# Performance work log

Measured on AMD Instinct MI355X. Metric: run time of the kernel, lower is better.

Reference implementation:

```python
import jax, jax.numpy as jnp
import numpy as np


def _qkernel(r, i, j, k):
    # Build the real-valued block kernel of a quaternion dense layer.
    # r,i,j,k: [in/4, out/4] -> kernel [in, out] implementing the Hamilton product.
    col_r = jnp.concatenate([r, -i, -j, -k], axis=0)
    col_i = jnp.concatenate([i, r, -k, j], axis=0)
    col_j = jnp.concatenate([j, k, r, -i], axis=0)
    col_k = jnp.concatenate([k, -j, i, r], axis=0)
    return jnp.concatenate([col_r, col_i, col_j, col_k], axis=1)


def setup_inputs() -> dict:
    key = jax.random.key(0)
    ks = jax.random.split(key, 12)
    B, F, H = 32768, 1024, 256
    F4, H4 = F // 4, H // 4
    s_in = 1.0 / np.sqrt(F)
    s_h = 1.0 / np.sqrt(H)
    inp = {
        "x": jax.random.normal(ks[0], (B, F), dtype=jnp.float32),
        "wx_r": jax.random.normal(ks[1], (4, F4, H4), dtype=jnp.float32) * s_in,
        "wx_i": jax.random.normal(ks[2], (4, F4, H4), dtype=jnp.float32) * s_in,
        "wx_j": jax.random.normal(ks[3], (4, F4, H4), dtype=jnp.float32) * s_in,
        "wx_k": jax.random.normal(ks[4], (4, F4, H4), dtype=jnp.float32) * s_in,
        "bx": jnp.zeros((4, H), dtype=jnp.float32),
        "uh_r": jax.random.normal(ks[5], (4, H4, H4), dtype=jnp.float32) * s_h,
        "uh_i": jax.random.normal(ks[6], (4, H4, H4), dtype=jnp.float32) * s_h,
        "uh_j": jax.random.normal(ks[7], (4, H4, H4), dtype=jnp.float32) * s_h,
        "uh_k": jax.random.normal(ks[8], (4, H4, H4), dtype=jnp.float32) * s_h,
        "fco_w": jax.random.normal(ks[9], (H, H), dtype=jnp.float32) * s_h,
        "fco_b": jnp.zeros((H,), dtype=jnp.float32),
    }
    return inp


def reference(x, wx_r, wx_i, wx_j, wx_k, bx, uh_r, uh_i, uh_j, uh_k, fco_w, fco_b):
    # Single-step quaternion LSTM cell with zero initial hidden/cell state.
    # Gate order along leading axis: [forget, input, output, cell].
    Kx = jax.vmap(_qkernel)(wx_r, wx_i, wx_j, wx_k)   # [4, F, H]
    Ku = jax.vmap(_qkernel)(uh_r, uh_i, uh_j, uh_k)   # [4, H, H]
    H = bx.shape[1]
    h0 = jnp.zeros((x.shape[0], H), dtype=x.dtype)
    c0 = h0
    gx = jnp.einsum('bf,gfh->gbh', x, Kx) + bx[:, None, :]   # [4, B, H]
    gu = jnp.einsum('bh,ghk->gbk', h0, Ku)                    # [4, B, H]
    z = gx + gu
    ft = jax.nn.sigmoid(z[0])
    it = jax.nn.sigmoid(z[1])
    ot = jax.nn.sigmoid(z[2])
    at = z[3]
    c = it * jnp.tanh(at) + ft * c0
    h = ot * jnp.tanh(c)
    return h @ fco_w + fco_b
```

## Files before the change

### kernel.cpp

```cpp
#include <hip/hip_runtime.h>
#include <cstdint>
#include <cstddef>

#define WS_WP   0
#define WS_FCO  1572864
#define WS_BP   1703936
#define WS_HVP  1707008

typedef __attribute__((ext_vector_type(8))) __bf16 bf16x8;
typedef __attribute__((ext_vector_type(4))) __bf16 bf16x4;
typedef __attribute__((ext_vector_type(4))) float floatx4;

__device__ __forceinline__ unsigned short f2bf(float f) {
  unsigned int u = __builtin_bit_cast(unsigned int, f);
  u += 0x7fffu + ((u >> 16) & 1u);
  return (unsigned short)(u >> 16);
}

__device__ __forceinline__ float sigmf(float z) {
  return __builtin_amdgcn_rcpf(1.f + __expf(-z));
}
__device__ __forceinline__ float tanh_(float z) {
  return 1.f - 2.f * __builtin_amdgcn_rcpf(1.f + __expf(2.f * z));
}

__device__ __forceinline__ void gld16(const void* g, void* l) {
  __builtin_amdgcn_global_load_lds(
      (const __attribute__((address_space(1))) unsigned int*)g,
      (__attribute__((address_space(3))) unsigned int*)l, 16, 0, 0);
}

__global__ __launch_bounds__(256) void pack_k(
    const float* __restrict__ wr, const float* __restrict__ wi,
    const float* __restrict__ wj, const float* __restrict__ wk,
    const float* __restrict__ bx, const float* __restrict__ fw,
    unsigned short* __restrict__ Wp, unsigned short* __restrict__ Fp,
    float* __restrict__ bp) {
  int t = threadIdx.x;
  if (blockIdx.x < 384) {
    int gpp = blockIdx.x >> 7;
    int oct = blockIdx.x & 127;
    int gp = gpp + 1;
    int h = t;
    int hb = h >> 6, hr = h & 63;
    int f0 = oct << 3;
    int fb = f0 >> 8, fr0 = f0 & 255;
    const int   comp_t[4][4] = {{0,1,2,3},{1,0,3,2},{2,3,0,1},{3,2,1,0}};
    const float sign_t[4][4] = {{1.f,-1.f,-1.f,-1.f},{1.f,1.f,-1.f,1.f},
                                {1.f,1.f,1.f,-1.f},{1.f,-1.f,1.f,1.f}};
    const float* srcs[4] = {wr, wi, wj, wk};
    const float* s = srcs[comp_t[hb][fb]] + ((size_t)((gp << 8) + fr0)) * 64 + hr;
    float sg = sign_t[hb][fb];
    unsigned short v[8];
#pragma unroll
    for (int j = 0; j < 8; ++j) v[j] = f2bf(sg * s[(size_t)j * 64]);
    int c = h * 3 + gpp;
    int cb = c / 192, nl = c % 192;
    int kb = oct >> 2, q = oct & 3;
    int idx16 = (nl << 2) + (q ^ ((nl >> 1) & 3));
    uint4 val = make_uint4(
        (unsigned)v[0] | ((unsigned)v[1] << 16), (unsigned)v[2] | ((unsigned)v[3] << 16),
        (unsigned)v[4] | ((unsigned)v[5] << 16), (unsigned)v[6] | ((unsigned)v[7] << 16));
    *(uint4*)(Wp + (size_t)(cb * 32 + kb) * 6144 + idx16 * 8) = val;
    if (oct == 0) bp[c] = bx[(gp << 8) + h];
  } else {
    int oct = blockIdx.x - 384;
    int n = t;
    int k0 = oct << 3;
    unsigned short v[8];
#pragma unroll
    for (int j = 0; j < 8; ++j) v[j] = f2bf(fw[(size_t)(k0 + j) * 256 + n]);
    int nb = n >> 7, nl = n & 127, kb = oct >> 2, q = oct & 3;
    int idx16 = (nl << 2) + (q ^ ((nl >> 1) & 3));
    uint4 val = make_uint4(
        (unsigned)v[0] | ((unsigned)v[1] << 16), (unsigned)v[2] | ((unsigned)v[3] << 16),
        (unsigned)v[4] | ((unsigned)v[5] << 16), (unsigned)v[6] | ((unsigned)v[7] << 16));
    *(uint4*)(Fp + (size_t)((nb << 3) + kb) * 4096 + idx16 * 8) = val;
  }
}

__global__ __launch_bounds__(512, 2) void gemm1_k(
    const float* __restrict__ x, const unsigned short* __restrict__ Wp,
    const float* __restrict__ bp, unsigned short* __restrict__ hvp) {
  __shared__ char smem[98304];
  float* zep = (float*)smem;

  const int t = threadIdx.x;
  const int lane = t & 63, wid = t >> 6;
  const int wm = wid >> 2, wn = wid & 3;
  const int lrow = lane & 15, q = lane >> 4;
  const int rowt = blockIdx.x;
  const int nbq = blockIdx.y;
  const int cb0 = nbq * 2;
  const int row0 = rowt * 128;
  const float* xbase = x + (size_t)row0 * 1024;

  const int m0 = t >> 3, kq = t & 7;
  const int sq8 = kq >> 1, shalf = kq & 1;

  floatx4 acc[4][6];
#pragma unroll
  for (int i = 0; i < 4; ++i)
#pragma unroll
    for (int j = 0; j < 6; ++j) acc[i][j] = (floatx4){0.f, 0.f, 0.f, 0.f};

#define STAGE_B(bufi, kt)                                                     \
  {                                                                           \
    unsigned short* sBs_ = (unsigned short*)(smem + (bufi) * 32768 + 8192);   \
    const unsigned short* bt0_ = Wp + ((size_t)cb0 * 32 + (kt)) * 6144;       \
    _Pragma("unroll")                                                         \
    for (int i_ = 0; i_ < 3; ++i_) {                                          \
      int s_ = t + i_ * 512;                                                  \
      int cbL_ = s_ >= 768;                                                   \
      const unsigned short* src_ =                                            \
          bt0_ + (size_t)cbL_ * 196608 + (s_ - cbL_ * 768) * 8;               \
      gld16(src_, sBs_ + s_ * 8);                                             \
    }                                                                         \
  }
#define LOAD_A(ra, kt)                                                        \
  {                                                                           \
    const float* ab_ = xbase + (size_t)m0 * 1024 + (kt) * 32 + kq * 4;        \
    ra[0] = *(const float4*)(ab_);                                            \
    ra[1] = *(const float4*)(ab_ + 64 * 1024);                                \
  }
#define WRITE_A(ra, bufi)                                                     \
  {                                                                           \
    unsigned short* sAs_ = (unsigned short*)(smem + (bufi) * 32768);          \
    _Pragma("unroll")                                                         \
    for (int i_ = 0; i_ < 2; ++i_) {                                          \
      int m_ = m0 + i_ * 64;                                                  \
      int slot_ = (m_ << 2) + (sq8 ^ ((m_ >> 1) & 3));                        \
      bf16x4 v_;                                                              \
      v_[0] = (__bf16)ra[i_].x; v_[1] = (__bf16)ra[i_].y;                     \
      v_[2] = (__bf16)ra[i_].z; v_[3] = (__bf16)ra[i_].w;                     \
      *(bf16x4*)(sAs_ + slot_ * 8 + shalf * 4) = v_;                          \
    }                                                                         \
  }
#define COMPUTE(bufi)                                                         \
  {                                                                           \
    const unsigned short* sA_ = (const unsigned short*)(smem + (bufi) * 32768);\
    const unsigned short* sB_ = sA_ + 4096;                                   \
    bf16x8 af[4], bf[6];                                                      \
    _Pragma("unroll")                                                         \
    for (int mt = 0; mt < 4; ++mt) {                                          \
      int m = wm * 64 + mt * 16 + lrow;                                       \
      int slot = (m << 2) + (q ^ ((m >> 1) & 3));                             \
      af[mt] = *(const bf16x8*)(const void*)(sA_ + slot * 8);                 \
    }                                                                         \
    _Pragma("unroll")                                                         \
    for (int nt = 0; nt < 6; ++nt) {                                          \
      int nl = (wn & 1) * 96 + nt * 16 + lrow;                                \
      int off16 = (nl << 2) + (q ^ ((nl >> 1) & 3));                          \
      bf[nt] = *(const bf16x8*)(const void*)(                                 \
          sB_ + ((size_t)(wn >> 1) * 768 + off16) * 8);                       \
    }                                                                         \
    _Pragma("unroll")                                                         \
    for (int mt = 0; mt < 4; ++mt)                                            \
      _Pragma("unroll")                                                       \
      for (int nt = 0; nt < 6; ++nt)                                          \
        acc[mt][nt] = __builtin_amdgcn_mfma_f32_16x16x32_bf16(                \
            af[mt], bf[nt], acc[mt][nt], 0, 0, 0);                            \
  }
#define BODY(kt, RC, RN)                                                      \
  {                                                                           \
    if ((kt) < 30) {                                                          \
      LOAD_A(RN, (kt) + 2)                                                    \
      STAGE_B(((kt) + 2) % 3, (kt) + 2)                                       \
    }                                                                         \
    COMPUTE((kt) % 3)                                                         \
    if ((kt) < 30) {                                                          \
      asm volatile("s_waitcnt vmcnt(5)" ::: "memory");                        \
    } else {                                                                  \
      asm volatile("s_waitcnt vmcnt(0)" ::: "memory");                        \
    }                                                                         \
    if ((kt) < 31) { WRITE_A(RC, ((kt) + 1) % 3) }                            \
    asm volatile("s_waitcnt lgkmcnt(0)" ::: "memory");                        \
    __builtin_amdgcn_s_barrier();                                             \
    asm volatile("" ::: "memory");                                            \
  }

  float4 raA[2], raB[2];
  LOAD_A(raA, 0)
  STAGE_B(0, 0)
  LOAD_A(raB, 1)
  STAGE_B(1, 1)
  WRITE_A(raA, 0)
  asm volatile("s_waitcnt vmcnt(5)" ::: "memory");
  asm volatile("s_waitcnt lgkmcnt(0)" ::: "memory");
  __builtin_amdgcn_s_barrier();
  asm volatile("" ::: "memory");

  for (int kt2 = 0; kt2 < 32; kt2 += 2) {
    BODY(kt2, raB, raA)
    BODY(kt2 + 1, raA, raB)
  }
#undef BODY
#undef COMPUTE
#undef STAGE_B
#undef LOAD_A
#undef WRITE_A
  __syncthreads();

  const float* bp0 = bp + cb0 * 192;
  const int er = t >> 4, oc = t & 15;
  const int cbL = oc >> 3, oo = oc & 7;
#pragma unroll
  for (int pass = 0; pass < 4; ++pass) {
    if (wm == (pass >> 1)) {
      int mtb = (pass & 1) * 2;
#pragma unroll
      for (int mi = 0; mi < 2; ++mi)
#pragma unroll
        for (int nt = 0; nt < 6; ++nt)
#pragma unroll
          for (int r = 0; r < 4; ++r)
            zep[(mi * 16 + q * 4 + r) * 385 + wn * 96 + nt * 16 + lrow] = acc[mtb + mi][nt][r];
    }
    __syncthreads();
    {
      int ml = pass * 32 + er;
      unsigned short v[8];
#pragma unroll
      for (int j = 0; j < 8; ++j) {
        int hl = oo * 8 + j;
        int cz = cbL * 192 + hl * 3;
        float zi = zep[er * 385 + cz + 0] + bp0[cz + 0];
        float zo = zep[er * 385 + cz + 1] + bp0[cz + 1];
        float zc = zep[er * 385 + cz + 2] + bp0[cz + 2];
        float it = sigmf(zi);
        float ot = sigmf(zo);
        float cc = it * tanh_(zc);
        v[j] = f2bf(ot * tanh_(cc));
      }
      int ktile = (cb0 + cbL) * 2 + (oo >> 2), qq = oo & 3;
      int idx16 = (ml << 2) + (qq ^ ((ml >> 1) & 3));
      uint4 val = make_uint4(
          (unsigned)v[0] | ((unsigned)v[1] << 16), (unsigned)v[2] | ((unsigned)v[3] << 16),
          (unsigned)v[4] | ((unsigned)v[5] << 16), (unsigned)v[6] | ((unsigned)v[7] << 16));
      *(uint4*)(hvp + (size_t)(rowt * 8 + ktile) * 4096 + idx16 * 8) = val;
    }
    __syncthreads();
  }
}

__global__ __launch_bounds__(256, 4) void gemm2_k(
    const unsigned short* __restrict__ hvp, const unsigned short* __restrict__ Fp,
    const float* __restrict__ fcob, float* __restrict__ out) {
  __shared__ unsigned short sB[32768];
  const int t = threadIdx.x;
  const int lane = t & 63, wid = t >> 6;
  const int wm = wid >> 1, wn = wid & 1;
  const int lrow = lane & 15, q = lane >> 4;
  const int mb = blockIdx.x, nb = blockIdx.y;

  const unsigned short* fpb = Fp + (size_t)nb * 32768;
#pragma unroll
  for (int i = 0; i < 16; ++i) gld16(fpb + (t + i * 256) * 8, sB + (t + i * 256) * 8);

  floatx4 acc[4][4];
#pragma unroll
  for (int i = 0; i < 4; ++i)
#pragma unroll
    for (int j = 0; j < 4; ++j) acc[i][j] = (floatx4){0.f, 0.f, 0.f, 0.f};
  __syncthreads();

#pragma unroll
  for (int kt = 0; kt < 8; ++kt) {
    const unsigned short* at_ = hvp + (size_t)(mb * 8 + kt) * 4096;
    bf16x8 af[4], bf[4];
#pragma unroll
    for (int mt = 0; mt < 4; ++mt) {
      int m = wm * 64 + mt * 16 + lrow;
      int o = (m << 2) + (q ^ ((m >> 1) & 3));
      af[mt] = *(const bf16x8*)(const void*)(at_ + o * 8);
    }
#pragma unroll
    for (int nt = 0; nt < 4; ++nt) {
      int n = wn * 64 + nt * 16 + lrow;
      int o = (n << 2) + (q ^ ((n >> 1) & 3));
      bf[nt] = *(const bf16x8*)(const void*)(sB + kt * 4096 + o * 8);
    }
#pragma unroll
    for (int mt = 0; mt < 4; ++mt)
#pragma unroll
      for (int nt = 0; nt < 4; ++nt)
        acc[mt][nt] = __builtin_amdgcn_mfma_f32_16x16x32_bf16(af[mt], bf[nt], acc[mt][nt], 0, 0, 0);
  }
#pragma unroll
  for (int nt = 0; nt < 4; ++nt) {
    int colg = nb * 128 + wn * 64 + nt * 16 + lrow;
    float bias = fcob[colg];
#pragma unroll
    for (int mt = 0; mt < 4; ++mt) {
      int rowg = mb * 128 + wm * 64 + mt * 16 + q * 4;
#pragma unroll
      for (int r = 0; r < 4; ++r)
        out[(size_t)(rowg + r) * 256 + colg] = acc[mt][nt][r] + bias;
    }
  }
}

extern "C" void kernel_launch(void* const* d_in, const int* in_sizes, int n_in,
                              void* d_out, int out_size, void* d_ws, size_t ws_size,
                              hipStream_t stream) {
  const float* x  = (const float*)d_in[0];
  const float* wr = (const float*)d_in[1];
  const float* wi = (const float*)d_in[2];
  const float* wj = (const float*)d_in[3];
  const float* wk = (const float*)d_in[4];
  const float* bx = (const float*)d_in[5];
  const float* fw = (const float*)d_in[10];
  const float* fb = (const float*)d_in[11];
  char* ws = (char*)d_ws;
  unsigned short* Wp  = (unsigned short*)(ws + WS_WP);
  unsigned short* Fp  = (unsigned short*)(ws + WS_FCO);
  float*          bp  = (float*)(ws + WS_BP);
  unsigned short* hvp = (unsigned short*)(ws + WS_HVP);
  float*          out = (float*)d_out;

  hipLaunchKernelGGL(pack_k,  dim3(416),    dim3(256), 0, stream, wr, wi, wj, wk, bx, fw, Wp, Fp, bp);
  hipLaunchKernelGGL(gemm1_k, dim3(256, 2), dim3(512), 0, stream, x, Wp, bp, hvp);
  hipLaunchKernelGGL(gemm2_k, dim3(256, 2), dim3(256), 0, stream, hvp, Fp, fb, out);
}
```

Measured before the change: 291.0 us.

## Split MFMA block into two halves interleaved with loads and priority barriers

Splits each k-step's 4x6 MFMA tile into two 4x3 halves. LDS reads of the second B half and the A write-back to shared memory are placed between the halves. Extra workgroup barriers, sched_barrier fences and s_setprio raise the priority of MFMA phases, so waves alternate between memory and compute phases in a ping-pong style. This aims to overlap LDS and global traffic with matrix work, at the cost of more barriers per iteration.

```diff
diff --git a/kernel.cpp b/kernel.cpp
--- a/kernel.cpp
+++ b/kernel.cpp
@@ -136,11 +136,14 @@
       *(bf16x4*)(sAs_ + slot_ * 8 + shalf * 4) = v_;                          \
     }                                                                         \
   }
-#define COMPUTE(bufi)                                                         \
+
+#define BODY(kt, RC, RN)                                                      \
   {                                                                           \
-    const unsigned short* sA_ = (const unsigned short*)(smem + (bufi) * 32768);\
+    const unsigned short* sA_ =                                               \
+        (const unsigned short*)(smem + ((kt) % 3) * 32768);                   \
     const unsigned short* sB_ = sA_ + 4096;                                   \
     bf16x8 af[4], bf[6];                                                      \
+                                  \
     _Pragma("unroll")                                                         \
     for (int mt = 0; mt < 4; ++mt) {                                          \
       int m = wm * 64 + mt * 16 + lrow;                                       \
@@ -148,35 +151,56 @@
       af[mt] = *(const bf16x8*)(const void*)(sA_ + slot * 8);                 \
     }                                                                         \
     _Pragma("unroll")                                                         \
-    for (int nt = 0; nt < 6; ++nt) {                                          \
+    for (int nt = 0; nt < 3; ++nt) {                                          \
       int nl = (wn & 1) * 96 + nt * 16 + lrow;                                \
       int off16 = (nl << 2) + (q ^ ((nl >> 1) & 3));                          \
       bf[nt] = *(const bf16x8*)(const void*)(                                 \
           sB_ + ((size_t)(wn >> 1) * 768 + off16) * 8);                       \
     }                                                                         \
-    _Pragma("unroll")                                                         \
-    for (int mt = 0; mt < 4; ++mt)                                            \
-      _Pragma("unroll")                                                       \
-      for (int nt = 0; nt < 6; ++nt)                                          \
-        acc[mt][nt] = __builtin_amdgcn_mfma_f32_16x16x32_bf16(                \
-            af[mt], bf[nt], acc[mt][nt], 0, 0, 0);                            \
-  }
-#define BODY(kt, RC, RN)                                                      \
-  {                                                                           \
     if ((kt) < 30) {                                                          \
       LOAD_A(RN, (kt) + 2)                                                    \
       STAGE_B(((kt) + 2) % 3, (kt) + 2)                                       \
     }                                                                         \
-    COMPUTE((kt) % 3)                                                         \
+    __builtin_amdgcn_s_barrier();                                             \
+    asm volatile("s_waitcnt lgkmcnt(0)" ::: "memory");                        \
+    __builtin_amdgcn_sched_barrier(0);                                        \
+    __builtin_amdgcn_s_setprio(1);                                            \
+    _Pragma("unroll")                                                         \
+    for (int mt = 0; mt < 4; ++mt)                                            \
+      _Pragma("unroll")                                                       \
+      for (int nt = 0; nt < 3; ++nt)                                          \
+        acc[mt][nt] = __builtin_amdgcn_mfma_f32_16x16x32_bf16(                \
+            af[mt], bf[nt], acc[mt][nt], 0, 0, 0);                            \
+    __builtin_amdgcn_s_setprio(0);                                            \
+    __builtin_amdgcn_sched_barrier(0);                                        \
+    __builtin_amdgcn_s_barrier();                                             \
+                  \
+    _Pragma("unroll")                                                         \
+    for (int nt = 3; nt < 6; ++nt) {                                          \
+      int nl = (wn & 1) * 96 + nt * 16 + lrow;                                \
+      int off16 = (nl << 2) + (q ^ ((nl >> 1) & 3));                          \
+      bf[nt] = *(const bf16x8*)(const void*)(                                 \
+          sB_ + ((size_t)(wn >> 1) * 768 + off16) * 8);                       \
+    }                                                                         \
     if ((kt) < 30) {                                                          \
       asm volatile("s_waitcnt vmcnt(5)" ::: "memory");                        \
     } else {                                                                  \
       asm volatile("s_waitcnt vmcnt(0)" ::: "memory");                        \
     }                                                                         \
     if ((kt) < 31) { WRITE_A(RC, ((kt) + 1) % 3) }                            \
+    __builtin_amdgcn_s_barrier();                                             \
     asm volatile("s_waitcnt lgkmcnt(0)" ::: "memory");                        \
+    __builtin_amdgcn_sched_barrier(0);                                        \
+    __builtin_amdgcn_s_setprio(1);                                            \
+    _Pragma("unroll")                                                         \
+    for (int mt = 0; mt < 4; ++mt)                                            \
+      _Pragma("unroll")                                                       \
+      for (int nt = 3; nt < 6; ++nt)                                          \
+        acc[mt][nt] = __builtin_amdgcn_mfma_f32_16x16x32_bf16(                \
+            af[mt], bf[nt], acc[mt][nt], 0, 0, 0);                            \
+    __builtin_amdgcn_s_setprio(0);                                            \
+    __builtin_amdgcn_sched_barrier(0);                                        \
     __builtin_amdgcn_s_barrier();                                             \
-    asm volatile("" ::: "memory");                                            \
   }
 
   float4 raA[2], raB[2];
@@ -195,7 +219,6 @@
     BODY(kt2 + 1, raA, raB)
   }
 #undef BODY
-#undef COMPUTE
 #undef STAGE_B
 #undef LOAD_A
 #undef WRITE_A
```

Measured after the change: 300.6 us. 3.3% more time.

## Halve gemm1 row tile to 64 and use double-buffered pipeline for higher occupancy

Applied to the files above, without the earlier changes.

Reduces the gemm1 block tile from 128 to 64 rows, doubling the grid to 512x2 blocks, and shrinks shared memory from 96KB to 56KB. The triple-buffered pipeline with manual waitcnt and barrier is replaced by a simple double buffer with __syncthreads. Launch bounds now request 4 blocks per CU, aiming for more latency hiding and better load balance across CUs. In exchange each block does less MFMA work per B-tile staged, so traffic on the packed weights doubles, and the prefetch distance drops from two tiles to one.

```diff
diff --git a/kernel.cpp b/kernel.cpp
--- a/kernel.cpp
+++ b/kernel.cpp
@@ -79,10 +79,10 @@
   }
 }
 
-__global__ __launch_bounds__(512, 2) void gemm1_k(
+__global__ __launch_bounds__(512, 4) void gemm1_k(
     const float* __restrict__ x, const unsigned short* __restrict__ Wp,
     const float* __restrict__ bp, unsigned short* __restrict__ hvp) {
-  __shared__ char smem[98304];
+  __shared__ char smem[57344];
   float* zep = (float*)smem;
 
   const int t = threadIdx.x;
@@ -92,21 +92,21 @@
   const int rowt = blockIdx.x;
   const int nbq = blockIdx.y;
   const int cb0 = nbq * 2;
-  const int row0 = rowt * 128;
+  const int row0 = rowt * 64;
   const float* xbase = x + (size_t)row0 * 1024;
 
-  const int m0 = t >> 3, kq = t & 7;
+  const int sr = t >> 3, kq = t & 7;
   const int sq8 = kq >> 1, shalf = kq & 1;
 
-  floatx4 acc[4][6];
-#pragma unroll
-  for (int i = 0; i < 4; ++i)
+  floatx4 acc[2][6];
+#pragma unroll
+  for (int i = 0; i < 2; ++i)
 #pragma unroll
     for (int j = 0; j < 6; ++j) acc[i][j] = (floatx4){0.f, 0.f, 0.f, 0.f};
 
 #define STAGE_B(bufi, kt)                                                     \
   {                                                                           \
-    unsigned short* sBs_ = (unsigned short*)(smem + (bufi) * 32768 + 8192);   \
+    unsigned short* sBs_ = (unsigned short*)(smem + (bufi) * 28672 + 4096);   \
     const unsigned short* bt0_ = Wp + ((size_t)cb0 * 32 + (kt)) * 6144;       \
     _Pragma("unroll")                                                         \
     for (int i_ = 0; i_ < 3; ++i_) {                                          \
@@ -118,32 +118,24 @@
     }                                                                         \
   }
 #define LOAD_A(ra, kt)                                                        \
-  {                                                                           \
-    const float* ab_ = xbase + (size_t)m0 * 1024 + (kt) * 32 + kq * 4;        \
-    ra[0] = *(const float4*)(ab_);                                            \
-    ra[1] = *(const float4*)(ab_ + 64 * 1024);                                \
-  }
+  { ra = *(const float4*)(xbase + (size_t)sr * 1024 + (kt) * 32 + kq * 4); }
 #define WRITE_A(ra, bufi)                                                     \
   {                                                                           \
-    unsigned short* sAs_ = (unsigned short*)(smem + (bufi) * 32768);          \
-    _Pragma("unroll")                                                         \
-    for (int i_ = 0; i_ < 2; ++i_) {                                          \
-      int m_ = m0 + i_ * 64;                                                  \
-      int slot_ = (m_ << 2) + (sq8 ^ ((m_ >> 1) & 3));                        \
-      bf16x4 v_;                                                              \
-      v_[0] = (__bf16)ra[i_].x; v_[1] = (__bf16)ra[i_].y;                     \
-      v_[2] = (__bf16)ra[i_].z; v_[3] = (__bf16)ra[i_].w;                     \
-      *(bf16x4*)(sAs_ + slot_ * 8 + shalf * 4) = v_;                          \
-    }                                                                         \
+    unsigned short* sAs_ = (unsigned short*)(smem + (bufi) * 28672);          \
+    int slot_ = (sr << 2) + (sq8 ^ ((sr >> 1) & 3));                          \
+    bf16x4 v_;                                                                \
+    v_[0] = (__bf16)ra.x; v_[1] = (__bf16)ra.y;                               \
+    v_[2] = (__bf16)ra.z; v_[3] = (__bf16)ra.w;                               \
+    *(bf16x4*)(sAs_ + slot_ * 8 + shalf * 4) = v_;                            \
   }
 #define COMPUTE(bufi)                                                         \
   {                                                                           \
-    const unsigned short* sA_ = (const unsigned short*)(smem + (bufi) * 32768);\
-    const unsigned short* sB_ = sA_ + 4096;                                   \
-    bf16x8 af[4], bf[6];                                                      \
-    _Pragma("unroll")                                                         \
-    for (int mt = 0; mt < 4; ++mt) {                                          \
-      int m = wm * 64 + mt * 16 + lrow;                                       \
+    const unsigned short* sA_ = (const unsigned short*)(smem + (bufi) * 28672);\
+    const unsigned short* sB_ = sA_ + 2048;                                   \
+    bf16x8 af[2], bf[6];                                                      \
+    _Pragma("unroll")                                                         \
+    for (int mt = 0; mt < 2; ++mt) {                                          \
+      int m = wm * 32 + mt * 16 + lrow;                                       \
       int slot = (m << 2) + (q ^ ((m >> 1) & 3));                             \
       af[mt] = *(const bf16x8*)(const void*)(sA_ + slot * 8);                 \
     }                                                                         \
@@ -155,70 +147,51 @@
           sB_ + ((size_t)(wn >> 1) * 768 + off16) * 8);                       \
     }                                                                         \
     _Pragma("unroll")                                                         \
-    for (int mt = 0; mt < 4; ++mt)                                            \
+    for (int mt = 0; mt < 2; ++mt)                                            \
       _Pragma("unroll")                                                       \
       for (int nt = 0; nt < 6; ++nt)                                          \
         acc[mt][nt] = __builtin_amdgcn_mfma_f32_16x16x32_bf16(                \
             af[mt], bf[nt], acc[mt][nt], 0, 0, 0);                            \
   }
-#define BODY(kt, RC, RN)                                                      \
-  {                                                                           \
-    if ((kt) < 30) {                                                          \
-      LOAD_A(RN, (kt) + 2)                                                    \
-      STAGE_B(((kt) + 2) % 3, (kt) + 2)                                       \
-    }                                                                         \
-    COMPUTE((kt) % 3)                                                         \
-    if ((kt) < 30) {                                                          \
-      asm volatile("s_waitcnt vmcnt(5)" ::: "memory");                        \
-    } else {                                                                  \
-      asm volatile("s_waitcnt vmcnt(0)" ::: "memory");                        \
-    }                                                                         \
-    if ((kt) < 31) { WRITE_A(RC, ((kt) + 1) % 3) }                            \
-    asm volatile("s_waitcnt lgkmcnt(0)" ::: "memory");                        \
-    __builtin_amdgcn_s_barrier();                                             \
-    asm volatile("" ::: "memory");                                            \
-  }
-
-  float4 raA[2], raB[2];
-  LOAD_A(raA, 0)
+
+  float4 ra;
+  LOAD_A(ra, 0)
   STAGE_B(0, 0)
-  LOAD_A(raB, 1)
-  STAGE_B(1, 1)
-  WRITE_A(raA, 0)
-  asm volatile("s_waitcnt vmcnt(5)" ::: "memory");
-  asm volatile("s_waitcnt lgkmcnt(0)" ::: "memory");
-  __builtin_amdgcn_s_barrier();
-  asm volatile("" ::: "memory");
-
-  for (int kt2 = 0; kt2 < 32; kt2 += 2) {
-    BODY(kt2, raB, raA)
-    BODY(kt2 + 1, raA, raB)
-  }
-#undef BODY
+  WRITE_A(ra, 0)
+  __syncthreads();
+
+  for (int kt = 0; kt < 32; ++kt) {
+    if (kt < 31) {
+      LOAD_A(ra, kt + 1)
+      STAGE_B((kt + 1) & 1, kt + 1)
+    }
+    COMPUTE(kt & 1)
+    if (kt < 31) WRITE_A(ra, (kt + 1) & 1)
+    __syncthreads();
+  }
 #undef COMPUTE
 #undef STAGE_B
 #undef LOAD_A
 #undef WRITE_A
-  __syncthreads();
 
   const float* bp0 = bp + cb0 * 192;
   const int er = t >> 4, oc = t & 15;
   const int cbL = oc >> 3, oo = oc & 7;
-#pragma unroll
-  for (int pass = 0; pass < 4; ++pass) {
-    if (wm == (pass >> 1)) {
-      int mtb = (pass & 1) * 2;
-#pragma unroll
-      for (int mi = 0; mi < 2; ++mi)
+  const int mb128 = rowt >> 1;
+#pragma unroll
+  for (int pass = 0; pass < 2; ++pass) {
+    if (wm == pass) {
+#pragma unroll
+      for (int mt = 0; mt < 2; ++mt)
 #pragma unroll
         for (int nt = 0; nt < 6; ++nt)
 #pragma unroll
           for (int r = 0; r < 4; ++r)
-            zep[(mi * 16 + q * 4 + r) * 385 + wn * 96 + nt * 16 + lrow] = acc[mtb + mi][nt][r];
+            zep[(mt * 16 + q * 4 + r) * 385 + wn * 96 + nt * 16 + lrow] = acc[mt][nt][r];
     }
     __syncthreads();
     {
-      int ml = pass * 32 + er;
+      int ml = (rowt & 1) * 64 + pass * 32 + er;
       unsigned short v[8];
 #pragma unroll
       for (int j = 0; j < 8; ++j) {
@@ -237,7 +210,7 @@
       uint4 val = make_uint4(
           (unsigned)v[0] | ((unsigned)v[1] << 16), (unsigned)v[2] | ((unsigned)v[3] << 16),
           (unsigned)v[4] | ((unsigned)v[5] << 16), (unsigned)v[6] | ((unsigned)v[7] << 16));
-      *(uint4*)(hvp + (size_t)(rowt * 8 + ktile) * 4096 + idx16 * 8) = val;
+      *(uint4*)(hvp + (size_t)(mb128 * 8 + ktile) * 4096 + idx16 * 8) = val;
     }
     __syncthreads();
   }
@@ -319,6 +292,6 @@
   float*          out = (float*)d_out;
 
   hipLaunchKernelGGL(pack_k,  dim3(416),    dim3(256), 0, stream, wr, wi, wj, wk, bx, fw, Wp, Fp, bp);
-  hipLaunchKernelGGL(gemm1_k, dim3(256, 2), dim3(512), 0, stream, x, Wp, bp, hvp);
+  hipLaunchKernelGGL(gemm1_k, dim3(512, 2), dim3(512), 0, stream, x, Wp, bp, hvp);
   hipLaunchKernelGGL(gemm2_k, dim3(256, 2), dim3(256), 0, stream, hvp, Fp, fb, out);
 }
```

Measured after the change: 292.0 us. About the same (+0.3%).
